# Kernel optimization log

Measured on AMD Instinct MI355X. Metric: run time of the kernel, lower is better.

The kernel has to match this reference:

```python
import jax, jax.numpy as jnp
import numpy as np

B, T, D, H, HD = 2, 2048, 1024, 16, 64


def setup_inputs() -> dict:
    key = jax.random.key(0)
    kx, kq, kk, kv, ko = jax.random.split(key, 5)
    s = 1.0 / np.sqrt(D)
    return {
        "x": jax.random.normal(kx, (B, T, D), dtype=jnp.float32),
        "Wq": jax.random.normal(kq, (H, D, HD), dtype=jnp.float32) * s,
        "Wk": jax.random.normal(kk, (H, D, HD), dtype=jnp.float32) * s,
        "Wv": jax.random.normal(kv, (H, D, HD), dtype=jnp.float32) * s,
        "Wo": jax.random.normal(ko, (D, D), dtype=jnp.float32) * s,
        "bo": jnp.zeros((D,), dtype=jnp.float32),
    }


def reference(x, Wq, Wk, Wv, Wo, bo):
    # Batched equivalent of the per-head loop: q/k/v for all heads at once.
    q = jnp.einsum("btd,hdk->bhtk", x, Wq)  # [B,H,T,HD]
    k = jnp.einsum("btd,hdk->bhtk", x, Wk)
    v = jnp.einsum("btd,hdk->bhtk", x, Wv)
    scale = 1.0 / jnp.sqrt(jnp.asarray(HD, dtype=x.dtype))
    scores = jnp.einsum("bhqk,bhsk->bhqs", q, k) * scale  # [B,H,T,T]
    causal = jnp.tril(jnp.ones((T, T), dtype=bool))
    scores = jnp.where(causal, scores, jnp.asarray(-1e9, dtype=scores.dtype))
    attn = jax.nn.softmax(scores, axis=-1)
    out = jnp.einsum("bhqs,bhsk->bhqk", attn, v)  # [B,H,T,HD]
    out = out.transpose(0, 2, 1, 3).reshape(B, T, H * HD)  # concat heads
    return out @ Wo + bo  # dropout is identity in eval (p used at train only)
```

## Files before the change

### kernel.cpp

```cpp
#include <hip/hip_runtime.h>
#include <hip/hip_bf16.h>
#include <stdint.h>
#include <stddef.h>

typedef __bf16 bf16_t;
typedef __attribute__((ext_vector_type(4))) __bf16 bf16x4;
typedef __attribute__((ext_vector_type(8))) __bf16 bf16x8;
typedef __attribute__((ext_vector_type(4))) float floatx4;

#define GLD16(gp, lp) __builtin_amdgcn_global_load_lds(                      \
    (__attribute__((address_space(1))) void*)(gp),                           \
    (__attribute__((address_space(3))) void*)(lp), 16, 0, 0)

__global__ __launch_bounds__(256) void prep(
    const float* __restrict__ x, const float* __restrict__ Wq,
    const float* __restrict__ Wk, const float* __restrict__ Wv,
    const float* __restrict__ Wo, bf16_t* __restrict__ XB,
    bf16_t* __restrict__ WT, bf16_t* __restrict__ WoT) {
  __shared__ bf16_t t[64][65];
  int bx = blockIdx.x;
  const int tid = threadIdx.x;
  if (bx < 2048) {
    const int i = (bx * 256 + tid) * 8;
    const float4 v0 = *(const float4*)(x + i);
    const float4 v1 = *(const float4*)(x + i + 4);
    bf16x8 o = {(bf16_t)v0.x, (bf16_t)v0.y, (bf16_t)v0.z, (bf16_t)v0.w,
                (bf16_t)v1.x, (bf16_t)v1.y, (bf16_t)v1.z, (bf16_t)v1.w};
    *(bf16x8*)(XB + i) = o;
    return;
  }
  bx -= 2048;
  const int g = tid >> 6, l = tid & 63;
  if (bx < 768) {
    const int d0 = (bx & 15) * 64, h = (bx >> 4) & 15, z = bx >> 8;
    const float* W = (z == 0) ? Wq : (z == 1) ? Wk : Wv;
    const float scl = (z == 0) ? 0.18033688011112042f : 1.0f;
    const float* src = W + (size_t)h * 65536 + (size_t)d0 * 64;
    #pragma unroll
    for (int i = 0; i < 16; ++i) { int r = g * 16 + i; t[r][l] = (bf16_t)(src[(size_t)r * 64 + l] * scl); }
    __syncthreads();
    bf16_t* dst = WT + ((size_t)z * 1024 + h * 64) * 1024 + d0;
    #pragma unroll
    for (int i = 0; i < 16; ++i) { int c = g * 16 + i; dst[(size_t)c * 1024 + l] = t[l][c]; }
  } else {
    bx -= 768;
    const int r0 = (bx & 15) * 64, c0 = (bx >> 4) * 64;
    #pragma unroll
    for (int i = 0; i < 16; ++i) { int r = g * 16 + i; t[r][l] = (bf16_t)Wo[(size_t)(r0 + r) * 1024 + c0 + l]; }
    __syncthreads();
    #pragma unroll
    for (int i = 0; i < 16; ++i) { int c = g * 16 + i; WoT[(size_t)(c0 + c) * 1024 + r0 + l] = t[l][c]; }
  }
}

template <bool BIAS, typename OutT>
__device__ __forceinline__ void gemm_body(
    const bf16_t* __restrict__ A, const bf16_t* __restrict__ Bt,
    OutT* __restrict__ C, const float* __restrict__ bias,
    int K, int lda, int ldb, int ldc, int m0, int n0,
    bf16_t* As, bf16_t* Bs) {
  const int tid = threadIdx.x;
  const int lane = tid & 63, w = tid >> 6;
  const int qd = lane >> 4, ln = lane & 15;
  const int wm = (w & 1) * 64, wn = (w >> 1) * 64;

  const floatx4 z4 = {0.f, 0.f, 0.f, 0.f};
  floatx4 acc[4][4];
  #pragma unroll
  for (int i = 0; i < 4; ++i)
    #pragma unroll
    for (int j = 0; j < 4; ++j) acc[i][j] = z4;

  for (int k0 = 0; k0 < K; k0 += 64) {
    #pragma unroll
    for (int i = 0; i < 4; ++i) {
      const int c = tid + i * 256;
      const int row = c >> 3;
      const int sg = (c & 7) ^ (row & 7);
      GLD16(A + (size_t)(m0 + row) * lda + k0 + sg * 8, As + (size_t)(w * 64 + i * 256) * 8);
      GLD16(Bt + (size_t)(n0 + row) * ldb + k0 + sg * 8, Bs + (size_t)(w * 64 + i * 256) * 8);
    }
    __syncthreads();
    #pragma unroll
    for (int h = 0; h < 2; ++h) {
      bf16x8 af[4], bfr[4];
      #pragma unroll
      for (int t = 0; t < 4; ++t) {
        const int ra = wm + t * 16 + ln;
        const int rb = wn + t * 16 + ln;
        af[t]  = *(const bf16x8*)(As + (size_t)ra * 64 + (((h * 4 + qd) ^ (ra & 7)) * 8));
        bfr[t] = *(const bf16x8*)(Bs + (size_t)rb * 64 + (((h * 4 + qd) ^ (rb & 7)) * 8));
      }
      #pragma unroll
      for (int mt = 0; mt < 4; ++mt)
        #pragma unroll
        for (int nt = 0; nt < 4; ++nt)
          acc[mt][nt] = __builtin_amdgcn_mfma_f32_16x16x32_bf16(af[mt], bfr[nt], acc[mt][nt], 0, 0, 0);
    }
    __syncthreads();
  }

  #pragma unroll
  for (int nt = 0; nt < 4; ++nt) {
    const int col = n0 + wn + nt * 16 + ln;
    const float bv = BIAS ? bias[col] : 0.f;
    #pragma unroll
    for (int mt = 0; mt < 4; ++mt) {
      const int row = m0 + wm + mt * 16 + qd * 4;
      #pragma unroll
      for (int r = 0; r < 4; ++r)
        C[(size_t)(row + r) * ldc + col] = (OutT)(acc[mt][nt][r] + bv);
    }
  }
}

__global__ __launch_bounds__(256) void proj_gemm(
    const bf16_t* __restrict__ XB, const bf16_t* __restrict__ WT,
    bf16_t* __restrict__ C1, bf16_t* __restrict__ VT) {
  __shared__ __align__(16) bf16_t As[128 * 64];
  __shared__ __align__(16) bf16_t Bs[128 * 64];
  int bx = blockIdx.x;
  if (bx < 512) {
    gemm_body<false, bf16_t>(XB, WT, C1, nullptr, 1024, 1024, 1024, 2048,
                             (bx & 31) * 128, (bx >> 5) * 128, As, Bs);
  } else {
    bx -= 512;
    gemm_body<false, bf16_t>(WT + (size_t)2048 * 1024, XB, VT, nullptr,
                             1024, 1024, 1024, 4096,
                             (bx & 7) * 128, (bx >> 3) * 128, As, Bs);
  }
}

__global__ __launch_bounds__(256) void out_gemm(
    const bf16_t* __restrict__ AO, const bf16_t* __restrict__ WoT,
    float* __restrict__ C, const float* __restrict__ bias) {
  __shared__ __align__(16) bf16_t As[128 * 64];
  __shared__ __align__(16) bf16_t Bs[128 * 64];
  gemm_body<true, float>(AO, WoT, C, bias, 1024, 1024, 1024, 1024,
                         blockIdx.x * 128, blockIdx.y * 128, As, Bs);
}

__global__ __launch_bounds__(256, 4) void flash_attn(
    const bf16_t* __restrict__ C1, const bf16_t* __restrict__ VT,
    bf16_t* __restrict__ AO) {
  __shared__ __align__(16) bf16_t Ks[2][64 * 64];
  __shared__ __align__(16) bf16_t Vs[2][64 * 64];
  __shared__ __align__(16) bf16_t Ps[4][16 * 64];

  const int bid = blockIdx.x;
  const int g = bid & 31;
  const int b = g >> 4, h = g & 15;
  const int v = bid >> 5, j = v & 7, sel = v >> 3;
  const int qt = (sel == 0) ? j : (sel == 1) ? 15 - j : (sel == 2) ? 16 + j : 31 - j;

  const int tid = threadIdx.x, lane = tid & 63, w = tid >> 6;
  const int qd = lane >> 4, ln = lane & 15;
  const bf16_t* Qb = C1 + (size_t)b * 2048 * 2048;

  bf16x8 qf0, qf1;
  {
    const bf16_t* qp = Qb + (size_t)(qt * 64 + w * 16 + ln) * 2048 + h * 64 + qd * 8;
    qf0 = *(const bf16x8*)qp;
    qf1 = *(const bf16x8*)(qp + 32);
  }
  const floatx4 z4 = {0.f, 0.f, 0.f, 0.f};
  floatx4 oacc[4];
  #pragma unroll
  for (int t = 0; t < 4; ++t) oacc[t] = z4;
  floatx4 osum = z4;
  const bf16_t one = (bf16_t)1.0f;
  const bf16x8 vone = {one, one, one, one, one, one, one, one};

  const bf16_t* Kg = Qb + 1024 + h * 64;
  const bf16_t* Vg = VT + (size_t)(h * 64) * 4096 + b * 2048;

  const int r0 = tid >> 3;
  const int g0 = ((tid & 7) ^ (r0 & 7)) * 8;

  auto STAGE = [&](int BUF, int SOFF) {
    GLD16(Kg + (size_t)(SOFF + r0) * 2048 + g0,      &Ks[BUF][w * 512]);
    GLD16(Kg + (size_t)(SOFF + r0 + 32) * 2048 + g0, &Ks[BUF][w * 512 + 2048]);
    GLD16(Vg + (size_t)r0 * 4096 + SOFF + g0,        &Vs[BUF][w * 512]);
    GLD16(Vg + (size_t)(r0 + 32) * 4096 + SOFF + g0, &Vs[BUF][w * 512 + 2048]);
  };

  STAGE(0, 0);

  const int e2 = (ln & 7) << 1;
  const int swf = qd ^ (ln & 7);

  for (int st = 0; st <= qt; ++st) {
    const int bi = st & 1;
    __syncthreads();
    if (st < qt) STAGE(bi ^ 1, (st + 1) * 64);

    floatx4 sa[4];
    __builtin_amdgcn_s_setprio(1);
    #pragma unroll
    for (int nt = 0; nt < 4; ++nt) {
      const bf16_t* kp = &Ks[bi][(nt * 16 + ln) * 64];
      bf16x8 kf0 = *(const bf16x8*)(kp + swf * 8);
      bf16x8 kf1 = *(const bf16x8*)(kp + (swf ^ 4) * 8);
      floatx4 t0 = z4;
      t0 = __builtin_amdgcn_mfma_f32_16x16x32_bf16(kf0, qf0, t0, 0, 0, 0);
      t0 = __builtin_amdgcn_mfma_f32_16x16x32_bf16(kf1, qf1, t0, 0, 0, 0);
      sa[nt] = t0;
    }
    __builtin_amdgcn_s_setprio(0);

    bf16x8 vf0[4], vf1[4];
    #pragma unroll
    for (int t = 0; t < 4; ++t) {
      const bf16_t* vp = &Vs[bi][(t * 16 + ln) * 64];
      vf0[t] = *(const bf16x8*)(vp + swf * 8);
      vf1[t] = *(const bf16x8*)(vp + (swf ^ 4) * 8);
    }

    #pragma unroll
    for (int nt = 0; nt < 4; ++nt) {
      float p[4];
      #pragma unroll
      for (int r = 0; r < 4; ++r) {
        float v2 = sa[nt][r];
        if (st == qt && (nt * 16 + qd * 4 + r) > (w * 16 + ln)) v2 = -1e30f;
        p[r] = __builtin_amdgcn_exp2f(v2);
      }
      bf16x4 pk = {(bf16_t)p[0], (bf16_t)p[1], (bf16_t)p[2], (bf16_t)p[3]};
      *(bf16x4*)(&Ps[w][ln * 64 + (((nt * 4 + qd) ^ e2) << 2)]) = pk;
    }
    bf16x8 pa0 = *(const bf16x8*)(&Ps[w][ln * 64 + ((((qd << 1)    ) ^ e2) << 2)]);
    bf16x8 pa1 = *(const bf16x8*)(&Ps[w][ln * 64 + ((((qd << 1) + 8) ^ e2) << 2)]);

    __builtin_amdgcn_s_setprio(1);
    #pragma unroll
    for (int t = 0; t < 4; ++t) {
      oacc[t] = __builtin_amdgcn_mfma_f32_16x16x32_bf16(pa0, vf0[t], oacc[t], 0, 0, 0);
      oacc[t] = __builtin_amdgcn_mfma_f32_16x16x32_bf16(pa1, vf1[t], oacc[t], 0, 0, 0);
    }
    osum = __builtin_amdgcn_mfma_f32_16x16x32_bf16(pa0, vone, osum, 0, 0, 0);
    osum = __builtin_amdgcn_mfma_f32_16x16x32_bf16(pa1, vone, osum, 0, 0, 0);
    __builtin_amdgcn_s_setprio(0);
  }

  #pragma unroll
  for (int r = 0; r < 4; ++r) {
    const float lr = 1.0f / osum[r];
    #pragma unroll
    for (int t = 0; t < 4; ++t) {
      const int col = h * 64 + t * 16 + ln;
      const int row = b * 2048 + qt * 64 + w * 16 + qd * 4 + r;
      AO[(size_t)row * 1024 + col] = (bf16_t)(oacc[t][r] * lr);
    }
  }
}

extern "C" void kernel_launch(void* const* d_in, const int* in_sizes, int n_in,
                              void* d_out, int out_size, void* d_ws, size_t ws_size,
                              hipStream_t stream) {
  const float* x  = (const float*)d_in[0];
  const float* Wq = (const float*)d_in[1];
  const float* Wk = (const float*)d_in[2];
  const float* Wv = (const float*)d_in[3];
  const float* Wo = (const float*)d_in[4];
  const float* bo = (const float*)d_in[5];
  float* out = (float*)d_out;

  bf16_t* WT  = (bf16_t*)d_ws;
  bf16_t* WoT = WT + (size_t)3072 * 1024;
  bf16_t* C1  = WoT + (size_t)1024 * 1024;
  bf16_t* AO  = C1 + (size_t)4096 * 2048;
  bf16_t* XB  = (bf16_t*)d_out;
  bf16_t* VT  = XB + (size_t)4096 * 1024;

  prep<<<dim3(3072), 256, 0, stream>>>(x, Wq, Wk, Wv, Wo, XB, WT, WoT);
  proj_gemm<<<dim3(768), 256, 0, stream>>>(XB, WT, C1, VT);
  flash_attn<<<dim3(1024), 256, 0, stream>>>(C1, VT, AO);
  out_gemm<<<dim3(32, 8), 256, 0, stream>>>(AO, WoT, out, bo);
}
```

Baseline: 169.2 us.

## Split long causal query tiles across two key ranges and merge in output GEMM

Query tiles in the second half of the sequence now have their key range split across two blocks. One block covers keys 0–15 and writes an unnormalized partial output plus row sums to scratch space reused from the weight buffers. The other covers the remaining keys and writes into AO. The output GEMM merges and normalizes the two partials while staging its A tile, for the M-blocks that need it. The aim is to shorten the longest causal blocks and balance work across the larger grid. The cost is extra scratch traffic and a synchronous, non-async A-tile load path in half of the output GEMM blocks.

```diff
diff --git a/kernel.cpp b/kernel.cpp
--- a/kernel.cpp
+++ b/kernel.cpp
@@ -53,12 +53,14 @@
   }
 }
 
-template <bool BIAS, typename OutT>
+template <bool BIAS, typename OutT, int AMODE>
 __device__ __forceinline__ void gemm_body(
     const bf16_t* __restrict__ A, const bf16_t* __restrict__ Bt,
     OutT* __restrict__ C, const float* __restrict__ bias,
     int K, int lda, int ldb, int ldc, int m0, int n0,
-    bf16_t* As, bf16_t* Bs) {
+    bf16_t* As, bf16_t* Bs,
+    const bf16_t* __restrict__ P0, const float* __restrict__ l0,
+    const float* __restrict__ l1) {
   const int tid = threadIdx.x;
   const int lane = tid & 63, w = tid >> 6;
   const int qd = lane >> 4, ln = lane & 15;
@@ -77,7 +79,21 @@
       const int c = tid + i * 256;
       const int row = c >> 3;
       const int sg = (c & 7) ^ (row & 7);
-      GLD16(A + (size_t)(m0 + row) * lda + k0 + sg * 8, As + (size_t)(w * 64 + i * 256) * 8);
+      if (AMODE == 0) {
+        GLD16(A + (size_t)(m0 + row) * lda + k0 + sg * 8, As + (size_t)(w * 64 + i * 256) * 8);
+      } else {
+        const int grow = m0 + row;
+        const int pr = ((grow >> 11) << 10) | (grow & 1023);
+        const int hh = k0 >> 6;
+        const float rv = 1.0f / (l0[pr * 16 + hh] + l1[pr * 16 + hh]);
+        const bf16x8 p1 = *(const bf16x8*)(A + (size_t)grow * lda + k0 + sg * 8);
+        const bf16x8 p0 = *(const bf16x8*)(P0 + (size_t)pr * 1024 + k0 + sg * 8);
+        bf16x8 mm;
+        #pragma unroll
+        for (int jj = 0; jj < 8; ++jj)
+          mm[jj] = (bf16_t)(((float)p0[jj] + (float)p1[jj]) * rv);
+        *(bf16x8*)(As + (size_t)c * 8) = mm;
+      }
       GLD16(Bt + (size_t)(n0 + row) * ldb + k0 + sg * 8, Bs + (size_t)(w * 64 + i * 256) * 8);
     }
     __syncthreads();
@@ -121,28 +137,39 @@
   __shared__ __align__(16) bf16_t Bs[128 * 64];
   int bx = blockIdx.x;
   if (bx < 512) {
-    gemm_body<false, bf16_t>(XB, WT, C1, nullptr, 1024, 1024, 1024, 2048,
-                             (bx & 31) * 128, (bx >> 5) * 128, As, Bs);
+    gemm_body<false, bf16_t, 0>(XB, WT, C1, nullptr, 1024, 1024, 1024, 2048,
+                                (bx & 31) * 128, (bx >> 5) * 128, As, Bs,
+                                nullptr, nullptr, nullptr);
   } else {
     bx -= 512;
-    gemm_body<false, bf16_t>(WT + (size_t)2048 * 1024, XB, VT, nullptr,
-                             1024, 1024, 1024, 4096,
-                             (bx & 7) * 128, (bx >> 3) * 128, As, Bs);
+    gemm_body<false, bf16_t, 0>(WT + (size_t)2048 * 1024, XB, VT, nullptr,
+                                1024, 1024, 1024, 4096,
+                                (bx & 7) * 128, (bx >> 3) * 128, As, Bs,
+                                nullptr, nullptr, nullptr);
   }
 }
 
 __global__ __launch_bounds__(256) void out_gemm(
     const bf16_t* __restrict__ AO, const bf16_t* __restrict__ WoT,
-    float* __restrict__ C, const float* __restrict__ bias) {
+    float* __restrict__ C, const float* __restrict__ bias,
+    const bf16_t* __restrict__ P0, const float* __restrict__ l0,
+    const float* __restrict__ l1) {
   __shared__ __align__(16) bf16_t As[128 * 64];
   __shared__ __align__(16) bf16_t Bs[128 * 64];
-  gemm_body<true, float>(AO, WoT, C, bias, 1024, 1024, 1024, 1024,
-                         blockIdx.x * 128, blockIdx.y * 128, As, Bs);
+  const int m0 = blockIdx.x * 128, n0 = blockIdx.y * 128;
+  if ((blockIdx.x >> 3) & 1) {
+    gemm_body<true, float, 1>(AO, WoT, C, bias, 1024, 1024, 1024, 1024,
+                              m0, n0, As, Bs, P0, l0, l1);
+  } else {
+    gemm_body<true, float, 0>(AO, WoT, C, bias, 1024, 1024, 1024, 1024,
+                              m0, n0, As, Bs, nullptr, nullptr, nullptr);
+  }
 }
 
 __global__ __launch_bounds__(256, 4) void flash_attn(
     const bf16_t* __restrict__ C1, const bf16_t* __restrict__ VT,
-    bf16_t* __restrict__ AO) {
+    bf16_t* __restrict__ AO, bf16_t* __restrict__ P0,
+    float* __restrict__ l0, float* __restrict__ l1) {
   __shared__ __align__(16) bf16_t Ks[2][64 * 64];
   __shared__ __align__(16) bf16_t Vs[2][64 * 64];
   __shared__ __align__(16) bf16_t Ps[4][16 * 64];
@@ -150,8 +177,15 @@
   const int bid = blockIdx.x;
   const int g = bid & 31;
   const int b = g >> 4, h = g & 15;
-  const int v = bid >> 5, j = v & 7, sel = v >> 3;
-  const int qt = (sel == 0) ? j : (sel == 1) ? 15 - j : (sel == 2) ? 16 + j : 31 - j;
+  const int v = bid >> 5;
+  int qt, s_lo, cm;
+  if (v < 16)           { qt = 16 + v; s_lo = 0;  cm = 1; }
+  else {
+    const int u = v - 16, m = u >> 1;
+    if ((u & 1) == 0)   { qt = 15 - m; s_lo = 0;  cm = 0; }
+    else                { qt = 31 - m; s_lo = 16; cm = 2; }
+  }
+  const int s_hi = (cm == 1) ? 15 : qt;
 
   const int tid = threadIdx.x, lane = tid & 63, w = tid >> 6;
   const int qd = lane >> 4, ln = lane & 15;
@@ -184,15 +218,15 @@
     GLD16(Vg + (size_t)(r0 + 32) * 4096 + SOFF + g0, &Vs[BUF][w * 512 + 2048]);
   };
 
-  STAGE(0, 0);
+  STAGE(0, s_lo * 64);
 
   const int e2 = (ln & 7) << 1;
   const int swf = qd ^ (ln & 7);
 
-  for (int st = 0; st <= qt; ++st) {
+  for (int st = s_lo; st <= s_hi; ++st) {
     const int bi = st & 1;
     __syncthreads();
-    if (st < qt) STAGE(bi ^ 1, (st + 1) * 64);
+    if (st < s_hi) STAGE(bi ^ 1, (st + 1) * 64);
 
     floatx4 sa[4];
     __builtin_amdgcn_s_setprio(1);
@@ -242,14 +276,31 @@
     __builtin_amdgcn_s_setprio(0);
   }
 
-  #pragma unroll
-  for (int r = 0; r < 4; ++r) {
-    const float lr = 1.0f / osum[r];
-    #pragma unroll
-    for (int t = 0; t < 4; ++t) {
-      const int col = h * 64 + t * 16 + ln;
-      const int row = b * 2048 + qt * 64 + w * 16 + qd * 4 + r;
-      AO[(size_t)row * 1024 + col] = (bf16_t)(oacc[t][r] * lr);
+  if (cm == 0) {
+    #pragma unroll
+    for (int r = 0; r < 4; ++r) {
+      const float lr = 1.0f / osum[r];
+      #pragma unroll
+      for (int t = 0; t < 4; ++t) {
+        const int col = h * 64 + t * 16 + ln;
+        const int row = b * 2048 + qt * 64 + w * 16 + qd * 4 + r;
+        AO[(size_t)row * 1024 + col] = (bf16_t)(oacc[t][r] * lr);
+      }
+    }
+  } else {
+    const int local = (qt - 16) * 64 + w * 16 + qd * 4;
+    bf16_t* Pw = (cm == 1)
+        ? P0 + (size_t)(b * 1024 + local) * 1024
+        : AO + (size_t)(b * 2048 + qt * 64 + w * 16 + qd * 4) * 1024;
+    float* lw = (cm == 1) ? l0 : l1;
+    #pragma unroll
+    for (int r = 0; r < 4; ++r) {
+      #pragma unroll
+      for (int t = 0; t < 4; ++t) {
+        const int col = h * 64 + t * 16 + ln;
+        Pw[(size_t)r * 1024 + col] = (bf16_t)oacc[t][r];
+      }
+      if (ln == 0) lw[(size_t)(b * 1024 + local + r) * 16 + h] = osum[r];
     }
   }
 }
@@ -272,8 +323,12 @@
   bf16_t* XB  = (bf16_t*)d_out;
   bf16_t* VT  = XB + (size_t)4096 * 1024;
 
+  bf16_t* P0 = WT;
+  float*  l0 = (float*)(WT + (size_t)2048 * 1024);
+  float*  l1 = l0 + (size_t)2048 * 16;
+
   prep<<<dim3(3072), 256, 0, stream>>>(x, Wq, Wk, Wv, Wo, XB, WT, WoT);
   proj_gemm<<<dim3(768), 256, 0, stream>>>(XB, WT, C1, VT);
-  flash_attn<<<dim3(1024), 256, 0, stream>>>(C1, VT, AO);
-  out_gemm<<<dim3(32, 8), 256, 0, stream>>>(AO, WoT, out, bo);
-}
+  flash_attn<<<dim3(1536), 256, 0, stream>>>(C1, VT, AO, P0, l0, l1);
+  out_gemm<<<dim3(32, 8), 256, 0, stream>>>(AO, WoT, out, bo, P0, l0, l1);
+}
```

Result: slower. 180.5 us (+6.7%).
